# Performance work log

Hardware: AMD Instinct MI355X
Metric: run time of the kernel (lower is better)

## Reference

```python
import jax, jax.numpy as jnp
import numpy as np

NI = 512
POSE_DIM = 128
IMG_SEQ = 1024
ATTN_CHANS = 64
NHEADS = NI // ATTN_CHANS  # 8
SCALE = float(np.sqrt(NI / NHEADS))  # sqrt(64) = 8
EPS = 1e-5


def _layernorm(x, g, b):
    m = jnp.mean(x, axis=-1, keepdims=True)
    v = jnp.var(x, axis=-1, keepdims=True)
    return (x - m) * jax.lax.rsqrt(v + EPS) * g + b


def setup_inputs() -> dict:
    key = jax.random.key(0)
    ks = jax.random.split(key, 8)
    w = lambda k, shape: (jax.random.normal(k, shape, dtype=jnp.float32) * 0.02)
    return {
        "x": jax.random.normal(ks[0], (8, NI, 32, 32), dtype=jnp.float32),
        "pose_embed": jax.random.normal(ks[1], (8, 2, POSE_DIM), dtype=jnp.float32),
        "norm_g": jnp.ones((NI,), jnp.float32),
        "norm_b": jnp.zeros((NI,), jnp.float32),
        "pnorm_g": jnp.ones((NI + 2,), jnp.float32),
        "pnorm_b": jnp.zeros((NI + 2,), jnp.float32),
        "pose_W": w(ks[2], (POSE_DIM, IMG_SEQ)),
        "pose_b": jnp.zeros((IMG_SEQ,), jnp.float32),
        "q_W": w(ks[3], (NI, NI)),
        "q_b": jnp.zeros((NI,), jnp.float32),
        "k_W": w(ks[4], (NI + 2, NI)),
        "k_b": jnp.zeros((NI,), jnp.float32),
        "v_W": w(ks[5], (NI + 2, NI)),
        "v_b": jnp.zeros((NI,), jnp.float32),
        "proj_W": w(ks[6], (NI, NI)),
        "proj_b": jnp.zeros((NI,), jnp.float32),
    }


def reference(x, pose_embed, norm_g, norm_b, pnorm_g, pnorm_b, pose_W, pose_b,
              q_W, q_b, k_W, k_b, v_W, v_b, proj_W, proj_b):
    n, c, h, w = x.shape
    s = h * w  # == IMG_SEQ
    xs = x.reshape(n, c, s).transpose(0, 2, 1)              # (n, s, c)
    pe = pose_embed @ pose_W + pose_b                        # (n, 2, s)
    pe = pe.transpose(0, 2, 1)                               # (n, s, 2)
    x_pose = jnp.concatenate([xs, pe], axis=2)               # (n, s, c+2)
    xn = _layernorm(xs, norm_g, norm_b)
    xpn = _layernorm(x_pose, pnorm_g, pnorm_b)
    q = xn @ q_W + q_b                                       # (n, s, c)
    k = xpn @ k_W + k_b
    v = xpn @ v_W + v_b
    # faithful to original: concat along feature dim, THEN split heads, THEN chunk
    qkv = jnp.concatenate([q, k, v], axis=-1)                # (n, s, 3c)
    qkv = qkv.reshape(n, s, NHEADS, 3 * ATTN_CHANS).transpose(0, 2, 1, 3)  # (n, H, s, 3d)
    q2 = qkv[..., :ATTN_CHANS]
    k2 = qkv[..., ATTN_CHANS:2 * ATTN_CHANS]
    v2 = qkv[..., 2 * ATTN_CHANS:]
    att = jnp.einsum('nhsd,nhtd->nhst', q2, k2) / SCALE      # (n, H, s, s)
    p = jax.nn.softmax(att, axis=-1)
    o = jnp.einsum('nhst,nhtd->nhsd', p, v2)                 # (n, H, s, d)
    o = o.transpose(0, 2, 1, 3).reshape(n, s, c)             # (n, s, c)
    o = o @ proj_W + proj_b
    o = o.transpose(0, 2, 1)                                 # (n, c, s)
    return o.reshape(n, c, h, w)
```

## Files before the change

kernel.cpp:

```cpp
#include <hip/hip_runtime.h>
#include <hip/hip_bf16.h>

typedef unsigned short u16;
typedef unsigned int u32;
typedef unsigned long long u64;
typedef __attribute__((ext_vector_type(8))) short short8;
typedef __attribute__((ext_vector_type(4))) short short4v;
typedef __attribute__((ext_vector_type(4))) float f32x4;

__device__ __forceinline__ u16 f2bf(float f) {
    union { float f; u32 u; } x; x.f = f;
    u32 r = x.u + 0x7fffu + ((x.u >> 16) & 1u);
    return (u16)(r >> 16);
}
__device__ __forceinline__ float fast_exp2(float x) {
#if __has_builtin(__builtin_amdgcn_exp2f)
    return __builtin_amdgcn_exp2f(x);
#else
    return exp2f(x);
#endif
}
__device__ __forceinline__ f32x4 mfma16(short4v a, short4v b, f32x4 c) {
#if __has_builtin(__builtin_amdgcn_mfma_f32_16x16x16bf16_1k)
    return __builtin_amdgcn_mfma_f32_16x16x16bf16_1k(a, b, c, 0, 0, 0);
#else
    asm("v_mfma_f32_16x16x16_bf16 %0, %1, %2, %0" : "+v"(c) : "v"(a), "v"(b));
    return c;
#endif
}

#define AS1C const __attribute__((address_space(1))) void*
#define AS3  __attribute__((address_space(3))) void*

__global__ __launch_bounds__(256) void pe_kernel(
    const float* __restrict__ pose, const float* __restrict__ poseW,
    const float* __restrict__ poseB, float* __restrict__ out)
{
    __shared__ float pr[128];
    int bj = blockIdx.x, tid = threadIdx.x;
    if (tid < 128) pr[tid] = pose[bj * 128 + tid];
    __syncthreads();
#pragma unroll
    for (int r = 0; r < 4; ++r) {
        int t = r * 256 + tid;
        float acc = poseB[t];
        for (int p = 0; p < 128; ++p)
            acc += pr[p] * poseW[p * 1024 + t];
        out[bj * 1024 + t] = acc;
    }
}

__global__ __launch_bounds__(512) void lnpack_kernel(
    const float* __restrict__ x, const float* __restrict__ pe,
    const float* __restrict__ ng, const float* __restrict__ nb,
    const float* __restrict__ pg, const float* __restrict__ pb,
    u16* __restrict__ xn, u16* __restrict__ xpn)
{
    __shared__ float tile[512 * 33];
    __shared__ float red[2][32][17];
    __shared__ float stats[6][32];
    int tid = threadIdx.x;
    int b = blockIdx.y, t0 = blockIdx.x * 32;
#pragma unroll
    for (int it = 0; it < 8; ++it) {
        int ch = it * 512 + tid;
        int c = ch >> 3, tc = (ch & 7) * 4;
        const float* gp = x + ((size_t)b * 512 + c) * 1024 + t0 + tc;
        float4 v = *(const float4*)gp;
        float* rowp = tile + c * 33 + tc;
        rowp[0] = v.x; rowp[1] = v.y; rowp[2] = v.z; rowp[3] = v.w;
    }
    __syncthreads();
    {
        int tl = tid & 31, cg = tid >> 5;
        float s = 0.f, sq = 0.f;
        for (int i = 0; i < 32; ++i) {
            int c = cg * 32 + i;
            float v = tile[c * 33 + tl];
            s += v; sq += v * v;
        }
        red[0][tl][cg] = s; red[1][tl][cg] = sq;
    }
    __syncthreads();
    if (tid < 32) {
        float S = 0.f, Q = 0.f;
        for (int g = 0; g < 16; ++g) { S += red[0][tid][g]; Q += red[1][tid][g]; }
        float m1 = S * (1.f / 512.f);
        float v1 = fmaxf(Q * (1.f / 512.f) - m1 * m1, 0.f);
        float r1 = rsqrtf(v1 + 1e-5f);
        float p0 = pe[(size_t)b * 2048 + t0 + tid];
        float p1 = pe[(size_t)b * 2048 + 1024 + t0 + tid];
        float S2 = S + p0 + p1, Q2 = Q + p0 * p0 + p1 * p1;
        float m2 = S2 * (1.f / 514.f);
        float v2 = fmaxf(Q2 * (1.f / 514.f) - m2 * m2, 0.f);
        float r2 = rsqrtf(v2 + 1e-5f);
        stats[0][tid] = m1; stats[1][tid] = r1; stats[2][tid] = m2;
        stats[3][tid] = r2; stats[4][tid] = p0; stats[5][tid] = p1;
    }
    __syncthreads();
    {
        int c = tid;
        float g1 = ng[c], b1 = nb[c];
        float g2 = pg[c], b2 = pb[c];
        for (int t = 0; t < 32; ++t) {
            float v = tile[c * 33 + t];
            int T = t0 + t;
            xn [((size_t)b * 1024 + T) * 512 + c] = f2bf((v - stats[0][t]) * stats[1][t] * g1 + b1);
            xpn[((size_t)b * 1024 + T) * 544 + c] = f2bf((v - stats[2][t]) * stats[3][t] * g2 + b2);
        }
        if (tid < 32) {
            float gg = (tid < 2) ? pg[512 + tid] : 0.f;
            float bbv = (tid < 2) ? pb[512 + tid] : 0.f;
            for (int t = 0; t < 32; ++t) {
                float val = 0.f;
                if (tid < 2)
                    val = (stats[4 + tid][t] - stats[2][t]) * stats[3][t] * gg + bbv;
                xpn[((size_t)b * 1024 + (t0 + t)) * 544 + 512 + tid] = f2bf(val);
            }
        }
    }
}

__global__ __launch_bounds__(256) void wtrans_kernel(
    const float* __restrict__ qW, const float* __restrict__ kW,
    const float* __restrict__ vW, const float* __restrict__ pW,
    u16* __restrict__ qWt, u16* __restrict__ kWt,
    u16* __restrict__ vWt, u16* __restrict__ pWt)
{
    int z = blockIdx.z;
    const float* src = (z == 0) ? qW : (z == 1) ? kW : (z == 2) ? vW : pW;
    u16* dst = (z == 0) ? qWt : (z == 1) ? kWt : (z == 2) ? vWt : pWt;
    int Kdim = (z == 1 || z == 2) ? 514 : 512;
    int Kpad = (z == 1 || z == 2) ? 544 : 512;
    int n0 = blockIdx.x * 32, k0 = blockIdx.y * 32;
    if (k0 >= Kpad) return;
    __shared__ float tt[32][33];
    int xx = threadIdx.x & 31, yy = threadIdx.x >> 5;
#pragma unroll
    for (int r = 0; r < 4; ++r) {
        int k = k0 + yy * 4 + r;
        tt[xx][yy * 4 + r] = (k < Kdim) ? src[(size_t)k * 512 + n0 + xx] : 0.f;
    }
    __syncthreads();
#pragma unroll
    for (int r = 0; r < 4; ++r) {
        int nl = yy * 4 + r;
        dst[(size_t)(n0 + nl) * Kpad + k0 + xx] = f2bf(tt[nl][xx]);
    }
}

#define BM 128
#define BN 64
#define BKK 32
#define QSCALE 0.18033688f
__global__ __launch_bounds__(256) void gemm_kernel(
    const u16* __restrict__ A, int lda,
    const u16* __restrict__ Bt, int ldb,
    const float* __restrict__ bias0, const float* __restrict__ bias1,
    int K, int mode, int coff,
    u16* __restrict__ oq, u16* __restrict__ ok, u16* __restrict__ ov,
    float* __restrict__ out32)
{
    __shared__ __align__(16) u16 As[BM * BKK];
    __shared__ __align__(16) u16 Bs[BN * BKK];
    const int tid = threadIdx.x;
    const int lane = tid & 63, w = tid >> 6;
    const int row0 = blockIdx.x * BM, col0 = blockIdx.y * BN;
    const int woffM = (w & 1) * 64, woffN = (w >> 1) * 32;
    const int lr = lane & 15, kg = lane >> 4;
    f32x4 acc[4][2] = {};
    for (int k0 = 0; k0 < K; k0 += BKK) {
#pragma unroll
        for (int h = 0; h < 3; ++h) {
            int c = tid + h * 256;
            if (c < 512) {
                int r = c >> 2, sl = c & 3;
                int kc = sl ^ (r & 3);
                __builtin_amdgcn_global_load_lds(
                    (AS1C)(A + (size_t)(row0 + r) * lda + k0 + kc * 8),
                    (AS3)(As + c * 8), 16, 0, 0);
            } else {
                int cB = c - 512;
                int r = cB >> 2, sl = cB & 3;
                int kc = sl ^ (r & 3);
                __builtin_amdgcn_global_load_lds(
                    (AS1C)(Bt + (size_t)(col0 + r) * ldb + k0 + kc * 8),
                    (AS3)(Bs + cB * 8), 16, 0, 0);
            }
        }
        __syncthreads();
        short8 af[4], bfr[2];
#pragma unroll
        for (int m = 0; m < 4; ++m) {
            int r = woffM + m * 16 + lr;
            af[m] = *(const short8*)(As + r * BKK + ((kg ^ (r & 3)) * 8));
        }
#pragma unroll
        for (int n = 0; n < 2; ++n) {
            int r = woffN + n * 16 + lr;
            bfr[n] = *(const short8*)(Bs + r * BKK + ((kg ^ (r & 3)) * 8));
        }
#pragma unroll
        for (int m = 0; m < 4; ++m)
#pragma unroll
            for (int n = 0; n < 2; ++n)
                acc[m][n] = __builtin_amdgcn_mfma_f32_16x16x32_bf16(af[m], bfr[n], acc[m][n], 0, 0, 0);
        __syncthreads();
    }
#pragma unroll
    for (int m = 0; m < 4; ++m) {
#pragma unroll
        for (int n = 0; n < 2; ++n) {
            int gcol = col0 + woffN + n * 16 + lr;
            float bv = (gcol < 512) ? bias0[gcol] : bias1[gcol - 512];
            int growb = row0 + woffM + m * 16 + kg * 4;
            int bb = growb >> 10, t0v = growb & 1023;
            float v0 = acc[m][n][0] + bv, v1 = acc[m][n][1] + bv;
            float v2 = acc[m][n][2] + bv, v3 = acc[m][n][3] + bv;
            if (mode == 0) {
                int cg = coff + gcol;
                int h = cg / 192;
                int rr = cg - h * 192;
                int role = rr >> 6, d = rr & 63;
                if (role == 0) { v0 *= QSCALE; v1 *= QSCALE; v2 *= QSCALE; v3 *= QSCALE; }
                if (role == 2) {
                    size_t base = ((((size_t)bb * 8 + h) * 64 + d) << 10) + t0v;
                    u64 pk = (u64)f2bf(v0) | ((u64)f2bf(v1) << 16)
                           | ((u64)f2bf(v2) << 32) | ((u64)f2bf(v3) << 48);
                    *(u64*)(ov + base) = pk;
                } else {
                    u16* o = role ? ok : oq;
                    size_t base = ((((size_t)bb * 8 + h) * 1024 + t0v) << 6) + d;
                    o[base]       = f2bf(v0);
                    o[base + 64]  = f2bf(v1);
                    o[base + 128] = f2bf(v2);
                    o[base + 192] = f2bf(v3);
                }
            } else {
                size_t base = (((size_t)bb * 512 + gcol) << 10) + t0v;
                float4 f4; f4.x = v0; f4.y = v1; f4.z = v2; f4.w = v3;
                *(float4*)(out32 + base) = f4;
            }
        }
    }
}

__global__ __launch_bounds__(256, 1) void attn_kernel(
    const u16* __restrict__ qb, const u16* __restrict__ kb,
    const u16* __restrict__ vt, u16* __restrict__ ob)
{
    __shared__ __align__(16) u16 Kl[2][4096];
    __shared__ __align__(16) u16 Vl[2][4096];
    int tid = threadIdx.x, lane = tid & 63, w = tid >> 6;
    int bid = blockIdx.x;
    int wid = (bid & 7) * 128 + (bid >> 3);
    int qt = wid & 15;
    int hh = (wid >> 4) & 7;
    int bbb = wid >> 7;
    int bh = bbb * 8 + hh;
    int q0 = qt * 64 + w * 16;
    int lr = lane & 15, kg = lane >> 4;
    const u16* qbase = qb + ((size_t)bh * 1024 + q0 + lr) * 64;
    short8 qf0 = *(const short8*)(qbase + kg * 8);
    short8 qf1 = *(const short8*)(qbase + 32 + kg * 8);
    f32x4 oT[4] = {};
    float lsum = 0.f;
    const u16* kbase = kb + (size_t)bh * 1024 * 64;
    const u16* vbase = vt + (size_t)bh * 64 * 1024;
    const int xr = lr & 7;
    const int vho = (kg & 1) * 4;
    const int vkg2 = kg >> 1;

#define STAGE(bf, s0) { \
    int g0 = tid, g1 = tid + 256; \
    { int r = g0 >> 3, cl = g0 & 7, cg = cl ^ (r & 7); \
      __builtin_amdgcn_global_load_lds((AS1C)(kbase + (size_t)((s0) + r) * 64 + cg * 8), \
                                       (AS3)(&Kl[bf][g0 * 8]), 16, 0, 0); } \
    { int r = g1 >> 3, cl = g1 & 7, cg = cl ^ (r & 7); \
      __builtin_amdgcn_global_load_lds((AS1C)(kbase + (size_t)((s0) + r) * 64 + cg * 8), \
                                       (AS3)(&Kl[bf][g1 * 8]), 16, 0, 0); } \
    { int d = g0 >> 3, cl = g0 & 7, cg = cl ^ (d & 7); \
      __builtin_amdgcn_global_load_lds((AS1C)(vbase + (size_t)d * 1024 + (s0) + cg * 8), \
                                       (AS3)(&Vl[bf][g0 * 8]), 16, 0, 0); } \
    { int d = g1 >> 3, cl = g1 & 7, cg = cl ^ (d & 7); \
      __builtin_amdgcn_global_load_lds((AS1C)(vbase + (size_t)d * 1024 + (s0) + cg * 8), \
                                       (AS3)(&Vl[bf][g1 * 8]), 16, 0, 0); } }

#define BODY(bf, st2) { \
    const u16* Kb = &Kl[bf][0]; \
    const u16* Vb = &Vl[bf][0]; \
    int rA = ((st2) * 32 + lr) * 64, rB = ((st2) * 32 + 16 + lr) * 64; \
    short8 k00 = *(const short8*)(Kb + rA + ((kg ^ xr) * 8)); \
    short8 k01 = *(const short8*)(Kb + rA + (((kg + 4) ^ xr) * 8)); \
    short8 k10 = *(const short8*)(Kb + rB + ((kg ^ xr) * 8)); \
    short8 k11 = *(const short8*)(Kb + rB + (((kg + 4) ^ xr) * 8)); \
    f32x4 sc0 = {}, sc1 = {}; \
    sc0 = __builtin_amdgcn_mfma_f32_16x16x32_bf16(k00, qf0, sc0, 0, 0, 0); \
    sc0 = __builtin_amdgcn_mfma_f32_16x16x32_bf16(k01, qf1, sc0, 0, 0, 0); \
    sc1 = __builtin_amdgcn_mfma_f32_16x16x32_bf16(k10, qf0, sc1, 0, 0, 0); \
    sc1 = __builtin_amdgcn_mfma_f32_16x16x32_bf16(k11, qf1, sc1, 0, 0, 0); \
    float p0 = fast_exp2(sc0[0]), p1 = fast_exp2(sc0[1]); \
    float p2 = fast_exp2(sc0[2]), p3 = fast_exp2(sc0[3]); \
    float p4 = fast_exp2(sc1[0]), p5 = fast_exp2(sc1[1]); \
    float p6 = fast_exp2(sc1[2]), p7 = fast_exp2(sc1[3]); \
    lsum += (((p0 + p1) + (p2 + p3)) + ((p4 + p5) + (p6 + p7))); \
    short4v pb0, pb1; \
    pb0[0] = (short)f2bf(p0); pb0[1] = (short)f2bf(p1); \
    pb0[2] = (short)f2bf(p2); pb0[3] = (short)f2bf(p3); \
    pb1[0] = (short)f2bf(p4); pb1[1] = (short)f2bf(p5); \
    pb1[2] = (short)f2bf(p6); pb1[3] = (short)f2bf(p7); \
    int c0 = ((((st2) * 4 + vkg2) ^ xr) * 8) + vho; \
    int c1 = ((((st2) * 4 + 2 + vkg2) ^ xr) * 8) + vho; \
    short4v va; \
    va = *(const short4v*)(Vb + (lr) * 64 + c0);       oT[0] = mfma16(va, pb0, oT[0]); \
    va = *(const short4v*)(Vb + (lr) * 64 + c1);       oT[0] = mfma16(va, pb1, oT[0]); \
    va = *(const short4v*)(Vb + (16 + lr) * 64 + c0);  oT[1] = mfma16(va, pb0, oT[1]); \
    va = *(const short4v*)(Vb + (16 + lr) * 64 + c1);  oT[1] = mfma16(va, pb1, oT[1]); \
    va = *(const short4v*)(Vb + (32 + lr) * 64 + c0);  oT[2] = mfma16(va, pb0, oT[2]); \
    va = *(const short4v*)(Vb + (32 + lr) * 64 + c1);  oT[2] = mfma16(va, pb1, oT[2]); \
    va = *(const short4v*)(Vb + (48 + lr) * 64 + c0);  oT[3] = mfma16(va, pb0, oT[3]); \
    va = *(const short4v*)(Vb + (48 + lr) * 64 + c1);  oT[3] = mfma16(va, pb1, oT[3]); }

    STAGE(0, 0)
    __syncthreads();
    for (int step = 0; step < 16; ++step) {
        int cur = step & 1;
        if (step < 15) STAGE(cur ^ 1, (step + 1) * 64)
        BODY(cur, 0)
        BODY(cur, 1)
        __syncthreads();
    }
#undef STAGE
#undef BODY

    float Z = lsum;
    Z += __shfl_xor(Z, 16);
    Z += __shfl_xor(Z, 32);
    float inv = 1.f / Z;
    u16* obase = ob + ((size_t)bbb * 1024 + q0 + lr) * 512 + hh * 64;
#pragma unroll
    for (int dt = 0; dt < 4; ++dt) {
        u32 lo = ((u32)f2bf(oT[dt][0] * inv)) | (((u32)f2bf(oT[dt][1] * inv)) << 16);
        u32 hi = ((u32)f2bf(oT[dt][2] * inv)) | (((u32)f2bf(oT[dt][3] * inv)) << 16);
        u32* dstp = (u32*)(obase + dt * 16 + kg * 4);
        dstp[0] = lo; dstp[1] = hi;
    }
}

extern "C" void kernel_launch(void* const* d_in, const int* in_sizes, int n_in,
                              void* d_out, int out_size, void* d_ws, size_t ws_size,
                              hipStream_t stream)
{
    (void)in_sizes; (void)n_in; (void)out_size;
    const float* x       = (const float*)d_in[0];
    const float* pose    = (const float*)d_in[1];
    const float* norm_g  = (const float*)d_in[2];
    const float* norm_b  = (const float*)d_in[3];
    const float* pnorm_g = (const float*)d_in[4];
    const float* pnorm_b = (const float*)d_in[5];
    const float* pose_W  = (const float*)d_in[6];
    const float* pose_b  = (const float*)d_in[7];
    const float* q_W     = (const float*)d_in[8];
    const float* q_b     = (const float*)d_in[9];
    const float* k_W     = (const float*)d_in[10];
    const float* k_b     = (const float*)d_in[11];
    const float* v_W     = (const float*)d_in[12];
    const float* v_b     = (const float*)d_in[13];
    const float* proj_W  = (const float*)d_in[14];
    const float* proj_b  = (const float*)d_in[15];
    float* out = (float*)d_out;

    if (ws_size < 44695552u) return;

    char* ws = (char*)d_ws;
    float* pe_ws = (float*)(ws);
    u16* xn    = (u16*)(ws + 65536);
    u16* xpn   = (u16*)(ws + 8454144);
    u16* qWt   = (u16*)(ws + 17367040);
    u16* kWt   = (u16*)(ws + 17891328);
    u16* vWt   = (u16*)(ws + 18448384);
    u16* pWt   = (u16*)(ws + 19005440);
    u16* qbuf  = (u16*)(ws + 19529728);
    u16* kbuf  = (u16*)(ws + 27918336);
    u16* vtb   = (u16*)(ws + 36306944);
    u16* obuf  = xn;

    hipLaunchKernelGGL(wtrans_kernel, dim3(16, 17, 4), dim3(256), 0, stream,
                       q_W, k_W, v_W, proj_W, qWt, kWt, vWt, pWt);
    hipLaunchKernelGGL(pe_kernel, dim3(16), dim3(256), 0, stream,
                       pose, pose_W, pose_b, pe_ws);
    hipLaunchKernelGGL(lnpack_kernel, dim3(32, 8), dim3(512), 0, stream,
                       x, pe_ws, norm_g, norm_b, pnorm_g, pnorm_b, xn, xpn);
    hipLaunchKernelGGL(gemm_kernel, dim3(64, 8), dim3(256), 0, stream,
                       xn, 512, qWt, 512, q_b, q_b, 512, 0, 0,
                       qbuf, kbuf, vtb, (float*)nullptr);
    hipLaunchKernelGGL(gemm_kernel, dim3(64, 16), dim3(256), 0, stream,
                       xpn, 544, kWt, 544, k_b, v_b, 544, 0, 512,
                       qbuf, kbuf, vtb, (float*)nullptr);
    hipLaunchKernelGGL(attn_kernel, dim3(1024), dim3(256), 0, stream,
                       qbuf, kbuf, vtb, obuf);
    hipLaunchKernelGGL(gemm_kernel, dim3(64, 8), dim3(256), 0, stream,
                       obuf, 512, pWt, 512, proj_b, proj_b, 512, 2, 0,
                       (u16*)nullptr, (u16*)nullptr, (u16*)nullptr, out);
}
```

Baseline: 115.7 us.

## Merge Q and KV GEMMs into one launch; attention processes two query tiles per wave

The separate Q and K/V projection GEMMs become a single kernel whose blocks pick their input and weight by blockIdx.y, which removes one launch and lets the two GEMMs share the GPU. The attention kernel now gives each wave two 16-row query tiles (128 queries per block, half as many blocks), so every K/V fragment read from LDS feeds twice the MFMA work. In exchange, register pressure in the attention kernel roughly doubles and the grid drops to 512 blocks, which may hurt occupancy or tail balance. The projection GEMM is simplified to a single fp32 output mode.

```diff
diff --git a/kernel.cpp b/kernel.cpp
--- a/kernel.cpp
+++ b/kernel.cpp
@@ -153,13 +153,102 @@
 #define BN 64
 #define BKK 32
 #define QSCALE 0.18033688f
+__global__ __launch_bounds__(256) void gemmqkv_kernel(
+    const u16* __restrict__ xnA, const u16* __restrict__ xpnA,
+    const u16* __restrict__ qWt, const u16* __restrict__ kWt,
+    const float* __restrict__ qB, const float* __restrict__ kB,
+    const float* __restrict__ vB,
+    u16* __restrict__ oq, u16* __restrict__ ok, u16* __restrict__ ov)
+{
+    __shared__ __align__(16) u16 As[BM * BKK];
+    __shared__ __align__(16) u16 Bs[BN * BKK];
+    const int tid = threadIdx.x;
+    const int lane = tid & 63, w = tid >> 6;
+    const bool isQ = (blockIdx.y < 8);
+    const u16* A  = isQ ? xnA : xpnA;
+    const u16* Bt = isQ ? qWt : kWt;
+    const int lda = isQ ? 512 : 544;
+    const int K   = lda;
+    const int row0 = blockIdx.x * BM;
+    const int col0 = blockIdx.y * BN;
+    const int colB0 = isQ ? col0 : col0 - 512;
+    const int woffM = (w & 1) * 64, woffN = (w >> 1) * 32;
+    const int lr = lane & 15, kg = lane >> 4;
+    f32x4 acc[4][2] = {};
+    for (int k0 = 0; k0 < K; k0 += BKK) {
+#pragma unroll
+        for (int h = 0; h < 3; ++h) {
+            int c = tid + h * 256;
+            if (c < 512) {
+                int r = c >> 2, sl = c & 3;
+                int kc = sl ^ (r & 3);
+                __builtin_amdgcn_global_load_lds(
+                    (AS1C)(A + (size_t)(row0 + r) * lda + k0 + kc * 8),
+                    (AS3)(As + c * 8), 16, 0, 0);
+            } else {
+                int cB = c - 512;
+                int r = cB >> 2, sl = cB & 3;
+                int kc = sl ^ (r & 3);
+                __builtin_amdgcn_global_load_lds(
+                    (AS1C)(Bt + (size_t)(colB0 + r) * lda + k0 + kc * 8),
+                    (AS3)(Bs + cB * 8), 16, 0, 0);
+            }
+        }
+        __syncthreads();
+        short8 af[4], bfr[2];
+#pragma unroll
+        for (int m = 0; m < 4; ++m) {
+            int r = woffM + m * 16 + lr;
+            af[m] = *(const short8*)(As + r * BKK + ((kg ^ (r & 3)) * 8));
+        }
+#pragma unroll
+        for (int n = 0; n < 2; ++n) {
+            int r = woffN + n * 16 + lr;
+            bfr[n] = *(const short8*)(Bs + r * BKK + ((kg ^ (r & 3)) * 8));
+        }
+#pragma unroll
+        for (int m = 0; m < 4; ++m)
+#pragma unroll
+            for (int n = 0; n < 2; ++n)
+                acc[m][n] = __builtin_amdgcn_mfma_f32_16x16x32_bf16(af[m], bfr[n], acc[m][n], 0, 0, 0);
+        __syncthreads();
+    }
+#pragma unroll
+    for (int m = 0; m < 4; ++m) {
+#pragma unroll
+        for (int n = 0; n < 2; ++n) {
+            int cg = col0 + woffN + n * 16 + lr;
+            float bv = (cg < 512) ? qB[cg] : ((cg < 1024) ? kB[cg - 512] : vB[cg - 1024]);
+            int growb = row0 + woffM + m * 16 + kg * 4;
+            int bb = growb >> 10, t0v = growb & 1023;
+            float v0 = acc[m][n][0] + bv, v1 = acc[m][n][1] + bv;
+            float v2 = acc[m][n][2] + bv, v3 = acc[m][n][3] + bv;
+            int h = cg / 192;
+            int rr = cg - h * 192;
+            int role = rr >> 6, d = rr & 63;
+            if (role == 0) { v0 *= QSCALE; v1 *= QSCALE; v2 *= QSCALE; v3 *= QSCALE; }
+            if (role == 2) {
+                size_t base = ((((size_t)bb * 8 + h) * 64 + d) << 10) + t0v;
+                u64 pk = (u64)f2bf(v0) | ((u64)f2bf(v1) << 16)
+                       | ((u64)f2bf(v2) << 32) | ((u64)f2bf(v3) << 48);
+                *(u64*)(ov + base) = pk;
+            } else {
+                u16* o = role ? ok : oq;
+                size_t base = ((((size_t)bb * 8 + h) * 1024 + t0v) << 6) + d;
+                o[base]       = f2bf(v0);
+                o[base + 64]  = f2bf(v1);
+                o[base + 128] = f2bf(v2);
+                o[base + 192] = f2bf(v3);
+            }
+        }
+    }
+}
+
 __global__ __launch_bounds__(256) void gemm_kernel(
     const u16* __restrict__ A, int lda,
     const u16* __restrict__ Bt, int ldb,
-    const float* __restrict__ bias0, const float* __restrict__ bias1,
-    int K, int mode, int coff,
-    u16* __restrict__ oq, u16* __restrict__ ok, u16* __restrict__ ov,
-    float* __restrict__ out32)
+    const float* __restrict__ bias0,
+    int K, float* __restrict__ out32)
 {
     __shared__ __align__(16) u16 As[BM * BKK];
     __shared__ __align__(16) u16 Bs[BN * BKK];
@@ -212,59 +301,41 @@
 #pragma unroll
         for (int n = 0; n < 2; ++n) {
             int gcol = col0 + woffN + n * 16 + lr;
-            float bv = (gcol < 512) ? bias0[gcol] : bias1[gcol - 512];
+            float bv = bias0[gcol];
             int growb = row0 + woffM + m * 16 + kg * 4;
             int bb = growb >> 10, t0v = growb & 1023;
-            float v0 = acc[m][n][0] + bv, v1 = acc[m][n][1] + bv;
-            float v2 = acc[m][n][2] + bv, v3 = acc[m][n][3] + bv;
-            if (mode == 0) {
-                int cg = coff + gcol;
-                int h = cg / 192;
-                int rr = cg - h * 192;
-                int role = rr >> 6, d = rr & 63;
-                if (role == 0) { v0 *= QSCALE; v1 *= QSCALE; v2 *= QSCALE; v3 *= QSCALE; }
-                if (role == 2) {
-                    size_t base = ((((size_t)bb * 8 + h) * 64 + d) << 10) + t0v;
-                    u64 pk = (u64)f2bf(v0) | ((u64)f2bf(v1) << 16)
-                           | ((u64)f2bf(v2) << 32) | ((u64)f2bf(v3) << 48);
-                    *(u64*)(ov + base) = pk;
-                } else {
-                    u16* o = role ? ok : oq;
-                    size_t base = ((((size_t)bb * 8 + h) * 1024 + t0v) << 6) + d;
-                    o[base]       = f2bf(v0);
-                    o[base + 64]  = f2bf(v1);
-                    o[base + 128] = f2bf(v2);
-                    o[base + 192] = f2bf(v3);
-                }
-            } else {
-                size_t base = (((size_t)bb * 512 + gcol) << 10) + t0v;
-                float4 f4; f4.x = v0; f4.y = v1; f4.z = v2; f4.w = v3;
-                *(float4*)(out32 + base) = f4;
-            }
+            size_t base = (((size_t)bb * 512 + gcol) << 10) + t0v;
+            float4 f4;
+            f4.x = acc[m][n][0] + bv; f4.y = acc[m][n][1] + bv;
+            f4.z = acc[m][n][2] + bv; f4.w = acc[m][n][3] + bv;
+            *(float4*)(out32 + base) = f4;
         }
     }
 }
 
 __global__ __launch_bounds__(256, 1) void attn_kernel(
-    const u16* __restrict__ qb, const u16* __restrict__ kb,
+    const u16* __restrict__ qg, const u16* __restrict__ kb,
     const u16* __restrict__ vt, u16* __restrict__ ob)
 {
     __shared__ __align__(16) u16 Kl[2][4096];
     __shared__ __align__(16) u16 Vl[2][4096];
     int tid = threadIdx.x, lane = tid & 63, w = tid >> 6;
     int bid = blockIdx.x;
-    int wid = (bid & 7) * 128 + (bid >> 3);
-    int qt = wid & 15;
-    int hh = (wid >> 4) & 7;
-    int bbb = wid >> 7;
+    int wid = (bid & 7) * 64 + (bid >> 3);
+    int qt = wid & 7;
+    int hh = (wid >> 3) & 7;
+    int bbb = wid >> 6;
     int bh = bbb * 8 + hh;
-    int q0 = qt * 64 + w * 16;
+    int q0 = qt * 128 + w * 16;
     int lr = lane & 15, kg = lane >> 4;
-    const u16* qbase = qb + ((size_t)bh * 1024 + q0 + lr) * 64;
-    short8 qf0 = *(const short8*)(qbase + kg * 8);
-    short8 qf1 = *(const short8*)(qbase + 32 + kg * 8);
-    f32x4 oT[4] = {};
-    float lsum = 0.f;
+    const u16* qbaseA = qg + ((size_t)bh * 1024 + q0 + lr) * 64;
+    const u16* qbaseB = qbaseA + 64 * 64;
+    short8 qa0 = *(const short8*)(qbaseA + kg * 8);
+    short8 qa1 = *(const short8*)(qbaseA + 32 + kg * 8);
+    short8 qc0 = *(const short8*)(qbaseB + kg * 8);
+    short8 qc1 = *(const short8*)(qbaseB + 32 + kg * 8);
+    f32x4 oTa[4] = {}, oTb[4] = {};
+    float lsa = 0.f, lsb = 0.f;
     const u16* kbase = kb + (size_t)bh * 1024 * 64;
     const u16* vbase = vt + (size_t)bh * 64 * 1024;
     const int xr = lr & 7;
@@ -294,32 +365,53 @@
     short8 k01 = *(const short8*)(Kb + rA + (((kg + 4) ^ xr) * 8)); \
     short8 k10 = *(const short8*)(Kb + rB + ((kg ^ xr) * 8)); \
     short8 k11 = *(const short8*)(Kb + rB + (((kg + 4) ^ xr) * 8)); \
-    f32x4 sc0 = {}, sc1 = {}; \
-    sc0 = __builtin_amdgcn_mfma_f32_16x16x32_bf16(k00, qf0, sc0, 0, 0, 0); \
-    sc0 = __builtin_amdgcn_mfma_f32_16x16x32_bf16(k01, qf1, sc0, 0, 0, 0); \
-    sc1 = __builtin_amdgcn_mfma_f32_16x16x32_bf16(k10, qf0, sc1, 0, 0, 0); \
-    sc1 = __builtin_amdgcn_mfma_f32_16x16x32_bf16(k11, qf1, sc1, 0, 0, 0); \
-    float p0 = fast_exp2(sc0[0]), p1 = fast_exp2(sc0[1]); \
-    float p2 = fast_exp2(sc0[2]), p3 = fast_exp2(sc0[3]); \
-    float p4 = fast_exp2(sc1[0]), p5 = fast_exp2(sc1[1]); \
-    float p6 = fast_exp2(sc1[2]), p7 = fast_exp2(sc1[3]); \
-    lsum += (((p0 + p1) + (p2 + p3)) + ((p4 + p5) + (p6 + p7))); \
-    short4v pb0, pb1; \
-    pb0[0] = (short)f2bf(p0); pb0[1] = (short)f2bf(p1); \
-    pb0[2] = (short)f2bf(p2); pb0[3] = (short)f2bf(p3); \
-    pb1[0] = (short)f2bf(p4); pb1[1] = (short)f2bf(p5); \
-    pb1[2] = (short)f2bf(p6); pb1[3] = (short)f2bf(p7); \
+    f32x4 sa0 = {}, sa1 = {}, sb0 = {}, sb1 = {}; \
+    sa0 = __builtin_amdgcn_mfma_f32_16x16x32_bf16(k00, qa0, sa0, 0, 0, 0); \
+    sa0 = __builtin_amdgcn_mfma_f32_16x16x32_bf16(k01, qa1, sa0, 0, 0, 0); \
+    sa1 = __builtin_amdgcn_mfma_f32_16x16x32_bf16(k10, qa0, sa1, 0, 0, 0); \
+    sa1 = __builtin_amdgcn_mfma_f32_16x16x32_bf16(k11, qa1, sa1, 0, 0, 0); \
+    sb0 = __builtin_amdgcn_mfma_f32_16x16x32_bf16(k00, qc0, sb0, 0, 0, 0); \
+    sb0 = __builtin_amdgcn_mfma_f32_16x16x32_bf16(k01, qc1, sb0, 0, 0, 0); \
+    sb1 = __builtin_amdgcn_mfma_f32_16x16x32_bf16(k10, qc0, sb1, 0, 0, 0); \
+    sb1 = __builtin_amdgcn_mfma_f32_16x16x32_bf16(k11, qc1, sb1, 0, 0, 0); \
+    float a0 = fast_exp2(sa0[0]), a1 = fast_exp2(sa0[1]); \
+    float a2 = fast_exp2(sa0[2]), a3 = fast_exp2(sa0[3]); \
+    float a4 = fast_exp2(sa1[0]), a5 = fast_exp2(sa1[1]); \
+    float a6 = fast_exp2(sa1[2]), a7 = fast_exp2(sa1[3]); \
+    float b0 = fast_exp2(sb0[0]), b1 = fast_exp2(sb0[1]); \
+    float b2 = fast_exp2(sb0[2]), b3 = fast_exp2(sb0[3]); \
+    float b4 = fast_exp2(sb1[0]), b5 = fast_exp2(sb1[1]); \
+    float b6 = fast_exp2(sb1[2]), b7 = fast_exp2(sb1[3]); \
+    lsa += (((a0 + a1) + (a2 + a3)) + ((a4 + a5) + (a6 + a7))); \
+    lsb += (((b0 + b1) + (b2 + b3)) + ((b4 + b5) + (b6 + b7))); \
+    short4v pa0, pa1, pc0, pc1; \
+    pa0[0] = (short)f2bf(a0); pa0[1] = (short)f2bf(a1); \
+    pa0[2] = (short)f2bf(a2); pa0[3] = (short)f2bf(a3); \
+    pa1[0] = (short)f2bf(a4); pa1[1] = (short)f2bf(a5); \
+    pa1[2] = (short)f2bf(a6); pa1[3] = (short)f2bf(a7); \
+    pc0[0] = (short)f2bf(b0); pc0[1] = (short)f2bf(b1); \
+    pc0[2] = (short)f2bf(b2); pc0[3] = (short)f2bf(b3); \
+    pc1[0] = (short)f2bf(b4); pc1[1] = (short)f2bf(b5); \
+    pc1[2] = (short)f2bf(b6); pc1[3] = (short)f2bf(b7); \
     int c0 = ((((st2) * 4 + vkg2) ^ xr) * 8) + vho; \
     int c1 = ((((st2) * 4 + 2 + vkg2) ^ xr) * 8) + vho; \
     short4v va; \
-    va = *(const short4v*)(Vb + (lr) * 64 + c0);       oT[0] = mfma16(va, pb0, oT[0]); \
-    va = *(const short4v*)(Vb + (lr) * 64 + c1);       oT[0] = mfma16(va, pb1, oT[0]); \
-    va = *(const short4v*)(Vb + (16 + lr) * 64 + c0);  oT[1] = mfma16(va, pb0, oT[1]); \
-    va = *(const short4v*)(Vb + (16 + lr) * 64 + c1);  oT[1] = mfma16(va, pb1, oT[1]); \
-    va = *(const short4v*)(Vb + (32 + lr) * 64 + c0);  oT[2] = mfma16(va, pb0, oT[2]); \
-    va = *(const short4v*)(Vb + (32 + lr) * 64 + c1);  oT[2] = mfma16(va, pb1, oT[2]); \
-    va = *(const short4v*)(Vb + (48 + lr) * 64 + c0);  oT[3] = mfma16(va, pb0, oT[3]); \
-    va = *(const short4v*)(Vb + (48 + lr) * 64 + c1);  oT[3] = mfma16(va, pb1, oT[3]); }
+    va = *(const short4v*)(Vb + (lr) * 64 + c0); \
+    oTa[0] = mfma16(va, pa0, oTa[0]);  oTb[0] = mfma16(va, pc0, oTb[0]); \
+    va = *(const short4v*)(Vb + (lr) * 64 + c1); \
+    oTa[0] = mfma16(va, pa1, oTa[0]);  oTb[0] = mfma16(va, pc1, oTb[0]); \
+    va = *(const short4v*)(Vb + (16 + lr) * 64 + c0); \
+    oTa[1] = mfma16(va, pa0, oTa[1]);  oTb[1] = mfma16(va, pc0, oTb[1]); \
+    va = *(const short4v*)(Vb + (16 + lr) * 64 + c1); \
+    oTa[1] = mfma16(va, pa1, oTa[1]);  oTb[1] = mfma16(va, pc1, oTb[1]); \
+    va = *(const short4v*)(Vb + (32 + lr) * 64 + c0); \
+    oTa[2] = mfma16(va, pa0, oTa[2]);  oTb[2] = mfma16(va, pc0, oTb[2]); \
+    va = *(const short4v*)(Vb + (32 + lr) * 64 + c1); \
+    oTa[2] = mfma16(va, pa1, oTa[2]);  oTb[2] = mfma16(va, pc1, oTb[2]); \
+    va = *(const short4v*)(Vb + (48 + lr) * 64 + c0); \
+    oTa[3] = mfma16(va, pa0, oTa[3]);  oTb[3] = mfma16(va, pc0, oTb[3]); \
+    va = *(const short4v*)(Vb + (48 + lr) * 64 + c1); \
+    oTa[3] = mfma16(va, pa1, oTa[3]);  oTb[3] = mfma16(va, pc1, oTb[3]); }
 
     STAGE(0, 0)
     __syncthreads();
@@ -333,16 +425,21 @@
 #undef STAGE
 #undef BODY
 
-    float Z = lsum;
-    Z += __shfl_xor(Z, 16);
-    Z += __shfl_xor(Z, 32);
-    float inv = 1.f / Z;
-    u16* obase = ob + ((size_t)bbb * 1024 + q0 + lr) * 512 + hh * 64;
+    float Za = lsa, Zb = lsb;
+    Za += __shfl_xor(Za, 16);  Za += __shfl_xor(Za, 32);
+    Zb += __shfl_xor(Zb, 16);  Zb += __shfl_xor(Zb, 32);
+    float inva = 1.f / Za, invb = 1.f / Zb;
+    u16* obaseA = ob + ((size_t)bbb * 1024 + q0 + lr) * 512 + hh * 64;
+    u16* obaseB = obaseA + (size_t)64 * 512;
 #pragma unroll
     for (int dt = 0; dt < 4; ++dt) {
-        u32 lo = ((u32)f2bf(oT[dt][0] * inv)) | (((u32)f2bf(oT[dt][1] * inv)) << 16);
-        u32 hi = ((u32)f2bf(oT[dt][2] * inv)) | (((u32)f2bf(oT[dt][3] * inv)) << 16);
-        u32* dstp = (u32*)(obase + dt * 16 + kg * 4);
+        u32 lo = ((u32)f2bf(oTa[dt][0] * inva)) | (((u32)f2bf(oTa[dt][1] * inva)) << 16);
+        u32 hi = ((u32)f2bf(oTa[dt][2] * inva)) | (((u32)f2bf(oTa[dt][3] * inva)) << 16);
+        u32* dstp = (u32*)(obaseA + dt * 16 + kg * 4);
+        dstp[0] = lo; dstp[1] = hi;
+        lo = ((u32)f2bf(oTb[dt][0] * invb)) | (((u32)f2bf(oTb[dt][1] * invb)) << 16);
+        hi = ((u32)f2bf(oTb[dt][2] * invb)) | (((u32)f2bf(oTb[dt][3] * invb)) << 16);
+        dstp = (u32*)(obaseB + dt * 16 + kg * 4);
         dstp[0] = lo; dstp[1] = hi;
     }
 }
@@ -391,15 +488,10 @@
                        pose, pose_W, pose_b, pe_ws);
     hipLaunchKernelGGL(lnpack_kernel, dim3(32, 8), dim3(512), 0, stream,
                        x, pe_ws, norm_g, norm_b, pnorm_g, pnorm_b, xn, xpn);
-    hipLaunchKernelGGL(gemm_kernel, dim3(64, 8), dim3(256), 0, stream,
-                       xn, 512, qWt, 512, q_b, q_b, 512, 0, 0,
-                       qbuf, kbuf, vtb, (float*)nullptr);
-    hipLaunchKernelGGL(gemm_kernel, dim3(64, 16), dim3(256), 0, stream,
-                       xpn, 544, kWt, 544, k_b, v_b, 544, 0, 512,
-                       qbuf, kbuf, vtb, (float*)nullptr);
-    hipLaunchKernelGGL(attn_kernel, dim3(1024), dim3(256), 0, stream,
+    hipLaunchKernelGGL(gemmqkv_kernel, dim3(64, 24), dim3(256), 0, stream,
+                       xn, xpn, qWt, kWt, q_b, k_b, v_b, qbuf, kbuf, vtb);
+    hipLaunchKernelGGL(attn_kernel, dim3(512), dim3(256), 0, stream,
                        qbuf, kbuf, vtb, obuf);
     hipLaunchKernelGGL(gemm_kernel, dim3(64, 8), dim3(256), 0, stream,
-                       obuf, 512, pWt, 512, proj_b, proj_b, 512, 2, 0,
-                       (u16*)nullptr, (u16*)nullptr, (u16*)nullptr, out);
-}
+                       obuf, 512, pWt, 512, proj_b, 512, out);
+}
```

Result: slower. 119.6 us (+3.5%).

## Double-buffer GEMM LDS tiles with BK=64 and a 32-wide K tail

Applied to the files above, without the earlier changes.

The GEMM kernel now uses two LDS buffers per operand and a K-step of 64 instead of 32. It issues the async global-to-LDS loads for the next tile before computing on the current one, so loads overlap MFMA work and there is one barrier per step instead of two. A 32-wide tail stage covers K values that are not a multiple of 64, such as the padded 514-row K/V weights. LDS use roughly quadruples, which may lower occupancy. The tail's swizzle layout must match the separate tail read path.

```diff
diff --git a/kernel.cpp b/kernel.cpp
--- a/kernel.cpp
+++ b/kernel.cpp
@@ -151,7 +151,6 @@
 
 #define BM 128
 #define BN 64
-#define BKK 32
 #define QSCALE 0.18033688f
 __global__ __launch_bounds__(256) void gemm_kernel(
     const u16* __restrict__ A, int lda,
@@ -161,52 +160,107 @@
     u16* __restrict__ oq, u16* __restrict__ ok, u16* __restrict__ ov,
     float* __restrict__ out32)
 {
-    __shared__ __align__(16) u16 As[BM * BKK];
-    __shared__ __align__(16) u16 Bs[BN * BKK];
+    __shared__ __align__(16) u16 As[2][BM * 64];
+    __shared__ __align__(16) u16 Bs[2][BN * 64];
     const int tid = threadIdx.x;
     const int lane = tid & 63, w = tid >> 6;
     const int row0 = blockIdx.x * BM, col0 = blockIdx.y * BN;
     const int woffM = (w & 1) * 64, woffN = (w >> 1) * 32;
     const int lr = lane & 15, kg = lane >> 4;
+    const int nfull = K >> 6;
+    const bool tail = (K & 63) != 0;
     f32x4 acc[4][2] = {};
-    for (int k0 = 0; k0 < K; k0 += BKK) {
-#pragma unroll
-        for (int h = 0; h < 3; ++h) {
-            int c = tid + h * 256;
-            if (c < 512) {
-                int r = c >> 2, sl = c & 3;
-                int kc = sl ^ (r & 3);
-                __builtin_amdgcn_global_load_lds(
-                    (AS1C)(A + (size_t)(row0 + r) * lda + k0 + kc * 8),
-                    (AS3)(As + c * 8), 16, 0, 0);
-            } else {
-                int cB = c - 512;
-                int r = cB >> 2, sl = cB & 3;
-                int kc = sl ^ (r & 3);
-                __builtin_amdgcn_global_load_lds(
-                    (AS1C)(Bt + (size_t)(col0 + r) * ldb + k0 + kc * 8),
-                    (AS3)(Bs + cB * 8), 16, 0, 0);
-            }
-        }
-        __syncthreads();
-        short8 af[4], bfr[2];
+
+#define STAGE64(bf, kk) { \
+    _Pragma("unroll") \
+    for (int h = 0; h < 6; ++h) { \
+        int c = tid + h * 256; \
+        if (c < 1024) { \
+            int r = c >> 3, sl = c & 7; \
+            int kc2 = sl ^ (r & 7); \
+            __builtin_amdgcn_global_load_lds( \
+                (AS1C)(A + (size_t)(row0 + r) * lda + (kk) + kc2 * 8), \
+                (AS3)(As[bf] + c * 8), 16, 0, 0); \
+        } else { \
+            int cB = c - 1024; \
+            int r = cB >> 3, sl = cB & 7; \
+            int kc2 = sl ^ (r & 7); \
+            __builtin_amdgcn_global_load_lds( \
+                (AS1C)(Bt + (size_t)(col0 + r) * ldb + (kk) + kc2 * 8), \
+                (AS3)(Bs[bf] + cB * 8), 16, 0, 0); \
+        } } }
+
+#define STAGE32(bf, kk) { \
+    _Pragma("unroll") \
+    for (int h = 0; h < 3; ++h) { \
+        int c = tid + h * 256; \
+        if (c < 512) { \
+            int r = c >> 2, sl = c & 3; \
+            int kc2 = sl ^ (r & 3); \
+            __builtin_amdgcn_global_load_lds( \
+                (AS1C)(A + (size_t)(row0 + r) * lda + (kk) + kc2 * 8), \
+                (AS3)(As[bf] + c * 8), 16, 0, 0); \
+        } else { \
+            int cB = c - 512; \
+            int r = cB >> 2, sl = cB & 3; \
+            int kc2 = sl ^ (r & 3); \
+            __builtin_amdgcn_global_load_lds( \
+                (AS1C)(Bt + (size_t)(col0 + r) * ldb + (kk) + kc2 * 8), \
+                (AS3)(Bs[bf] + cB * 8), 16, 0, 0); \
+        } } }
+
+    STAGE64(0, 0)
+    __syncthreads();
+    int buf = 0;
+    for (int step = 0; step < nfull; ++step) {
+        int knext = (step + 1) << 6;
+        if (step + 1 < nfull) { STAGE64(buf ^ 1, knext) }
+        else if (tail)        { STAGE32(buf ^ 1, knext) }
+        short8 af[4][2], bfr[2][2];
 #pragma unroll
         for (int m = 0; m < 4; ++m) {
             int r = woffM + m * 16 + lr;
-            af[m] = *(const short8*)(As + r * BKK + ((kg ^ (r & 3)) * 8));
+            const u16* base = As[buf] + r * 64;
+            af[m][0] = *(const short8*)(base + ((kg ^ (r & 7)) * 8));
+            af[m][1] = *(const short8*)(base + (((kg + 4) ^ (r & 7)) * 8));
         }
 #pragma unroll
         for (int n = 0; n < 2; ++n) {
             int r = woffN + n * 16 + lr;
-            bfr[n] = *(const short8*)(Bs + r * BKK + ((kg ^ (r & 3)) * 8));
+            const u16* base = Bs[buf] + r * 64;
+            bfr[n][0] = *(const short8*)(base + ((kg ^ (r & 7)) * 8));
+            bfr[n][1] = *(const short8*)(base + (((kg + 4) ^ (r & 7)) * 8));
+        }
+#pragma unroll
+        for (int m = 0; m < 4; ++m)
+#pragma unroll
+            for (int n = 0; n < 2; ++n) {
+                acc[m][n] = __builtin_amdgcn_mfma_f32_16x16x32_bf16(af[m][0], bfr[n][0], acc[m][n], 0, 0, 0);
+                acc[m][n] = __builtin_amdgcn_mfma_f32_16x16x32_bf16(af[m][1], bfr[n][1], acc[m][n], 0, 0, 0);
+            }
+        __syncthreads();
+        buf ^= 1;
+    }
+    if (tail) {
+        short8 af[4], bfr[2];
+#pragma unroll
+        for (int m = 0; m < 4; ++m) {
+            int r = woffM + m * 16 + lr;
+            af[m] = *(const short8*)(As[buf] + r * 32 + ((kg ^ (r & 3)) * 8));
+        }
+#pragma unroll
+        for (int n = 0; n < 2; ++n) {
+            int r = woffN + n * 16 + lr;
+            bfr[n] = *(const short8*)(Bs[buf] + r * 32 + ((kg ^ (r & 3)) * 8));
         }
 #pragma unroll
         for (int m = 0; m < 4; ++m)
 #pragma unroll
             for (int n = 0; n < 2; ++n)
                 acc[m][n] = __builtin_amdgcn_mfma_f32_16x16x32_bf16(af[m], bfr[n], acc[m][n], 0, 0, 0);
-        __syncthreads();
-    }
+    }
+#undef STAGE64
+#undef STAGE32
 #pragma unroll
     for (int m = 0; m < 4; ++m) {
 #pragma unroll
```

Measured after the change: 115.9 us. Within noise of the previous version (+0.3%).
